# Performance work log

Measured on AMD Instinct MI355X. Metric: run time of the kernel, lower is better.

## Reference

```python
import jax, jax.numpy as jnp
import numpy as np

NEURONS = 512
CHANNELS = 384
H, W = 13, 13
BATCH = 512


def setup_inputs() -> dict:
    key = jax.random.key(0)
    kx, ks, kd, kb = jax.random.split(key, 4)
    x = jax.random.normal(kx, (BATCH, CHANNELS, H, W), dtype=jnp.float32)
    W_s = jax.random.normal(ks, (NEURONS, H, W), dtype=jnp.float32)      # spatial readout per neuron
    W_d = jax.random.normal(kd, (NEURONS, CHANNELS), dtype=jnp.float32)  # channel readout (squeezed 1x1 conv kernel)
    W_b = jax.random.normal(kb, (1, NEURONS), dtype=jnp.float32)
    return {"x": x, "W_s": W_s, "W_d": W_d, "W_b": W_b}


def reference(x, W_s, W_d, W_b):
    # Original: out = einsum('bchw,nhw->bnchw') -> per-neuron 1x1 conv with W_d[n] -> sum over (c,h,w) -> + W_b
    # Mathematically: out[b,n] = sum_{c,h,w} x[b,c,h,w] * W_s[n,h,w] * W_d[n,c] + W_b[0,n]
    # Factorized into two contractions, avoiding the (b,n,c,h,w) intermediate.
    pooled = jnp.einsum('bchw,nhw->bnc', x, W_s)   # spatial weighted pooling: [B, N, C]
    out = jnp.einsum('bnc,nc->bn', pooled, W_d)    # channel readout: [B, N]
    return out + W_b
```

## Files before the change

kernel.cpp:

```cpp
#include <hip/hip_runtime.h>


#define B_   512
#define C_   384
#define N_   512
#define HW_  169
#define CT   128
#define SXR  200

#define WSF_ELEMS  ((size_t)32 * 6 * 64 * 8)
#define WDF_ELEMS  ((size_t)24 * 32 * 64 * 4)
#define PART_ELEMS ((size_t)3 * B_ * N_)

typedef __bf16 bf16x8 __attribute__((ext_vector_type(8)));
typedef float f32x4  __attribute__((ext_vector_type(4)));
typedef float f32x4u __attribute__((ext_vector_type(4), aligned(4)));
typedef unsigned u32x4 __attribute__((ext_vector_type(4)));

__device__ __forceinline__ __bf16 f2bf(float f) {
  union { float f; unsigned u; } v; v.f = f;
  unsigned r = (v.u + 0x7FFFu + ((v.u >> 16) & 1u)) >> 16;
  unsigned short s = (unsigned short)r;
  return __builtin_bit_cast(__bf16, s);
}

__device__ __forceinline__ unsigned pack_trunc(float a, float b) {
  return __builtin_amdgcn_perm(__builtin_bit_cast(unsigned, b),
                               __builtin_bit_cast(unsigned, a), 0x07060302u);
}

__global__ __launch_bounds__(256)
void prep_aux_kernel(const float* __restrict__ Ws,
                     const float* __restrict__ Wd,
                     __bf16* __restrict__ wsf,
                     float* __restrict__ wdf) {
  int t = blockIdx.x * 256 + threadIdx.x;
  if (t < 12288) {
    int lane = t & 63;
    int fr   = t >> 6;
    int kb   = fr % 6;
    int nm   = fr / 6;
    int n    = nm * 16 + (lane & 15);
    int k0   = kb * 32 + (lane >> 4) * 8;
    const float* src = Ws + (size_t)n * HW_;
    bf16x8 v;
    #pragma unroll
    for (int j = 0; j < 8; ++j) {
      int k = k0 + j;
      float f = (k < HW_) ? src[k] : 0.f;
      v[j] = f2bf(f);
    }
    *(bf16x8*)(wsf + (size_t)t * 8) = v;
  } else {
    int t2 = t - 12288;
    int lane = t2 & 63;
    int fr   = t2 >> 6;
    int nm   = fr & 31;
    int cm   = fr >> 5;
    int n    = nm * 16 + (lane & 15);
    int c0   = cm * 16 + (lane >> 4) * 4;
    f32x4 w = *(const f32x4u*)(Wd + (size_t)n * C_ + c0);
    *(f32x4*)(wdf + (size_t)t2 * 4) = w;
  }
}

__global__ __launch_bounds__(256, 4)
void conv_part(const float* __restrict__ x,
               const __bf16* __restrict__ wsf,
               const float* __restrict__ wdf,
               float* __restrict__ part) {
  __shared__ float red[4 * 512];

  const int tid  = threadIdx.x;
  const int id    = blockIdx.x;
  const int slot  = id & 7;
  const int t8    = id >> 3;
  const int c_blk = t8 % 3;
  const int b     = (t8 / 3) * 8 + slot;

  const int lane  = tid & 63;
  const int wv    = tid >> 6;
  const int lrow  = lane & 15;
  const int lquad = lane >> 4;

  bf16x8 a[2][6];
  #pragma unroll
  for (int mi = 0; mi < 2; ++mi) {
    const float* rp = x + ((size_t)b * C_ + (size_t)c_blk * CT + wv * 32 + mi * 16 + lrow) * HW_;
    #pragma unroll
    for (int kb = 0; kb < 6; ++kb) {
      const int k0 = kb * 32 + lquad * 8;
      float v0, v1, v2, v3, v4, v5, v6, v7;
      if (kb < 5 || k0 + 7 < HW_) {
        f32x4u t0 = *(const f32x4u*)(rp + k0);
        f32x4u t1 = *(const f32x4u*)(rp + k0 + 4);
        v0 = t0[0]; v1 = t0[1]; v2 = t0[2]; v3 = t0[3];
        v4 = t1[0]; v5 = t1[1]; v6 = t1[2]; v7 = t1[3];
      } else {
        v0 = (k0 + 0 < HW_) ? rp[k0 + 0] : 0.f;
        v1 = v2 = v3 = v4 = v5 = v6 = v7 = 0.f;
      }
      u32x4 pk;
      pk.x = pack_trunc(v0, v1);
      pk.y = pack_trunc(v2, v3);
      pk.z = pack_trunc(v4, v5);
      pk.w = pack_trunc(v6, v7);
      a[mi][kb] = __builtin_bit_cast(bf16x8, pk);
    }
  }

  const int cm0 = c_blk * 8 + wv * 2;
  const __bf16* bb = wsf + (size_t)lane * 8;
  const float*  wb = wdf + (size_t)lane * 4;
  const f32x4 zero = {0.f, 0.f, 0.f, 0.f};

  #pragma unroll 1
  for (int nf = 0; nf < 32; ++nf) {
    bf16x8 bfr[6];
    #pragma unroll
    for (int kb = 0; kb < 6; ++kb)
      bfr[kb] = *(const bf16x8*)(bb + ((size_t)nf * 6 + kb) * 512);

    f32x4 acc[2] = {zero, zero};
    #pragma unroll
    for (int kb = 0; kb < 6; ++kb)
      #pragma unroll
      for (int mi = 0; mi < 2; ++mi)
        acc[mi] = __builtin_amdgcn_mfma_f32_16x16x32_bf16(
            a[mi][kb], bfr[kb], acc[mi], 0, 0, 0);

    float t = 0.f;
    #pragma unroll
    for (int mi = 0; mi < 2; ++mi) {
      const f32x4 w = *(const f32x4*)(wb + (((size_t)(cm0 + mi) * 32 + nf) * 256));
      t += acc[mi][0] * w[0] + acc[mi][1] * w[1]
         + acc[mi][2] * w[2] + acc[mi][3] * w[3];
    }
    t += __shfl_xor(t, 16, 64);
    t += __shfl_xor(t, 32, 64);
    if (lane < 16)
      red[wv * 512 + nf * 16 + lrow] = t;
  }
  __syncthreads();

  float* pb = part + ((size_t)c_blk * B_ + b) * N_;
  #pragma unroll
  for (int r = 0; r < 2; ++r) {
    const int n = r * 256 + tid;
    float v = red[n] + red[512 + n] + red[1024 + n] + red[1536 + n];
    pb[n] = v;
  }
}

__global__ __launch_bounds__(256)
void reduce_part(const float* __restrict__ part,
                 const float* __restrict__ Wb,
                 float* __restrict__ out) {
  const size_t S = (size_t)B_ * N_;
  int idx = (blockIdx.x * 256 + threadIdx.x) * 4;
  f32x4 a0 = *(const f32x4u*)(part + idx);
  f32x4 a1 = *(const f32x4u*)(part + S + idx);
  f32x4 a2 = *(const f32x4u*)(part + 2 * S + idx);
  f32x4 wb = *(const f32x4u*)(Wb + (idx & (N_ - 1)));
  f32x4 r;
  #pragma unroll
  for (int i = 0; i < 4; ++i)
    r[i] = a0[i] + a1[i] + a2[i] + wb[i];
  *(f32x4*)(out + idx) = r;
}

__global__ __launch_bounds__(256, 3)
void conv_fused_v8(const float* __restrict__ x,
                   const __bf16* __restrict__ wsf,
                   const float* __restrict__ wdf,
                   const float* __restrict__ Wb,
                   float* __restrict__ out) {
  __shared__ __align__(16) __bf16 Xs[CT * SXR];
  __shared__ float red[4][64];

  const int tid  = threadIdx.x;
  const int id    = blockIdx.x;
  const int slot  = id & 7;
  const int t8    = id >> 3;
  const int c_blk = t8 % 3;
  const int b     = (t8 / 3) * 8 + slot;

  const int lane  = tid & 63;
  const int wv    = tid >> 6;
  const int cq    = (wv >> 1) * 64;
  const int nq    = (wv & 1) * 64;
  const int lrow  = lane & 15;
  const int lquad = lane >> 4;

  const float* src = x + ((size_t)b * C_ + (size_t)c_blk * CT) * HW_;
  #pragma unroll 4
  for (int p = 0; p < 24; ++p) {
    int i   = p * 256 + tid;
    int row = i / 48;
    int ch  = i - row * 48;
    const float* bp = src + row * HW_ + ch * 4;
    float v0 = 0.f, v1 = 0.f, v2 = 0.f, v3 = 0.f;
    if (ch < 42) {
      f32x4u t = *(const f32x4u*)bp;
      v0 = t[0]; v1 = t[1]; v2 = t[2]; v3 = t[3];
    } else if (ch == 42) {
      v0 = bp[0];
    }
    unsigned d0 = pack_trunc(v0, v1);
    unsigned d1 = pack_trunc(v2, v3);
    uint2 d; d.x = d0; d.y = d1;
    *(uint2*)&Xs[row * SXR + ch * 4] = d;
  }
  __syncthreads();

  const int cm0 = c_blk * 8 + (cq >> 4);

  #pragma unroll 1
  for (int nb = 0; nb < 4; ++nb) {
    const int nm0 = nb * 8 + (nq >> 4);
    const __bf16* bbase = wsf + ((size_t)nm0 * 6) * 512 + (size_t)lane * 8;

    const f32x4 zero = {0.f, 0.f, 0.f, 0.f};
    f32x4 acc[4][4];
    #pragma unroll
    for (int mi = 0; mi < 4; ++mi)
      #pragma unroll
      for (int ni = 0; ni < 4; ++ni)
        acc[mi][ni] = zero;

    #pragma unroll
    for (int kb = 0; kb < 6; ++kb) {
      bf16x8 afr[4], bfr[4];
      #pragma unroll
      for (int mi = 0; mi < 4; ++mi)
        afr[mi] = *(const bf16x8*)&Xs[(cq + mi * 16 + lrow) * SXR + kb * 32 + lquad * 8];
      #pragma unroll
      for (int ni = 0; ni < 4; ++ni)
        bfr[ni] = *(const bf16x8*)(bbase + ((size_t)ni * 6 + kb) * 512);
      #pragma unroll
      for (int mi = 0; mi < 4; ++mi)
        #pragma unroll
        for (int ni = 0; ni < 4; ++ni)
          acc[mi][ni] = __builtin_amdgcn_mfma_f32_16x16x32_bf16(
              afr[mi], bfr[ni], acc[mi][ni], 0, 0, 0);
    }

    float s[4] = {0.f, 0.f, 0.f, 0.f};
    #pragma unroll
    for (int ni = 0; ni < 4; ++ni) {
      #pragma unroll
      for (int mi = 0; mi < 4; ++mi) {
        const f32x4 w = *(const f32x4*)(wdf +
            (((size_t)(cm0 + mi) * 32 + (nm0 + ni)) * 64 + lane) * 4);
        s[ni] += acc[mi][ni][0] * w[0] + acc[mi][ni][1] * w[1]
               + acc[mi][ni][2] * w[2] + acc[mi][ni][3] * w[3];
      }
    }

    #pragma unroll
    for (int ni = 0; ni < 4; ++ni) {
      s[ni] += __shfl_xor(s[ni], 16, 64);
      s[ni] += __shfl_xor(s[ni], 32, 64);
    }
    if (lane < 16) {
      #pragma unroll
      for (int ni = 0; ni < 4; ++ni)
        red[wv][ni * 16 + lrow] = s[ni];
    }
    __syncthreads();

    if (tid < 128) {
      const int half = tid >> 6;
      const int idx  = tid & 63;
      const int n    = nb * 128 + tid;
      float v = red[half][idx] + red[half + 2][idx];
      if (c_blk == 0) v += Wb[n];
      atomicAdd(&out[(size_t)b * N_ + n], v);
    }
    __syncthreads();
  }
}


#define LDSS 104
#define KCH  96
#define NT   128

__global__ __launch_bounds__(256)
void conv_main_fallback(const float* __restrict__ x,
                        const float* __restrict__ Ws_g,
                        const float* __restrict__ Wd,
                        const float* __restrict__ Wb,
                        float* __restrict__ out) {
  __shared__ __align__(16) __bf16 Xs[CT][LDSS];
  __shared__ __align__(16) __bf16 Ws[NT][LDSS];

  const int tid   = threadIdx.x;
  const int n_blk = blockIdx.x;
  const int c_blk = blockIdx.y;
  const int b     = blockIdx.z;
  const int c0 = c_blk * CT;
  const int n0 = n_blk * NT;
  const int lane  = tid & 63;
  const int wv    = tid >> 6;
  const int cq    = (wv >> 1) * 64;
  const int nq    = (wv & 1) * 64;
  const int lrow  = lane & 15;
  const int lquad = lane >> 4;

  const f32x4 zero = {0.f, 0.f, 0.f, 0.f};
  f32x4 acc[4][4];
  #pragma unroll
  for (int mi = 0; mi < 4; ++mi)
    #pragma unroll
    for (int ni = 0; ni < 4; ++ni)
      acc[mi][ni] = zero;

  const float* xb  = x    + (size_t)b  * (C_ * HW_) + (size_t)c0 * HW_;
  const float* wsb = Ws_g + (size_t)n0 * HW_;

  for (int ch = 0; ch < 2; ++ch) {
    const int k0 = ch * KCH;
    __syncthreads();
    for (int e = tid; e < CT * KCH; e += 256) {
      int r   = e / KCH;
      int col = e - r * KCH;
      int k   = k0 + col;
      float vx = 0.f, vw = 0.f;
      if (k < HW_) {
        vx = xb [r * HW_ + k];
        vw = wsb[r * HW_ + k];
      }
      Xs[r][col] = f2bf(vx);
      Ws[r][col] = f2bf(vw);
    }
    __syncthreads();

    #pragma unroll
    for (int ks = 0; ks < 3; ++ks) {
      const int kc = ks * 32 + lquad * 8;
      bf16x8 afr[4], bfr[4];
      #pragma unroll
      for (int mi = 0; mi < 4; ++mi)
        afr[mi] = *(const bf16x8*)&Xs[cq + mi * 16 + lrow][kc];
      #pragma unroll
      for (int ni = 0; ni < 4; ++ni)
        bfr[ni] = *(const bf16x8*)&Ws[nq + ni * 16 + lrow][kc];
      #pragma unroll
      for (int mi = 0; mi < 4; ++mi)
        #pragma unroll
        for (int ni = 0; ni < 4; ++ni)
          acc[mi][ni] = __builtin_amdgcn_mfma_f32_16x16x32_bf16(
              afr[mi], bfr[ni], acc[mi][ni], 0, 0, 0);
    }
  }

  #pragma unroll
  for (int ni = 0; ni < 4; ++ni) {
    const int n = n0 + nq + ni * 16 + lrow;
    float sv = 0.f;
    #pragma unroll
    for (int mi = 0; mi < 4; ++mi) {
      const int cbase = c0 + cq + mi * 16 + lquad * 4;
      #pragma unroll
      for (int i = 0; i < 4; ++i)
        sv += acc[mi][ni][i] * Wd[(size_t)n * C_ + (cbase + i)];
    }
    sv += __shfl_xor(sv, 16, 64);
    sv += __shfl_xor(sv, 32, 64);
    if (lane < 16) {
      if (c_blk == 0 && cq == 0) sv += Wb[n];
      atomicAdd(&out[(size_t)b * N_ + n], sv);
    }
  }
}

extern "C" void kernel_launch(void* const* d_in, const int* in_sizes, int n_in,
                              void* d_out, int out_size, void* d_ws, size_t ws_size,
                              hipStream_t stream) {
  const float* x   = (const float*)d_in[0];
  const float* Wsp = (const float*)d_in[1];
  const float* Wd  = (const float*)d_in[2];
  const float* Wb  = (const float*)d_in[3];
  float* out = (float*)d_out;

  const size_t need_basic = WSF_ELEMS * sizeof(__bf16) + WDF_ELEMS * sizeof(float);
  const size_t need_full  = need_basic + PART_ELEMS * sizeof(float);

  if (ws_size >= need_full) {
    __bf16* wsf  = (__bf16*)d_ws;
    float*  wdf  = (float*)(wsf + WSF_ELEMS);
    float*  partb = wdf + WDF_ELEMS;

    prep_aux_kernel<<<240, 256, 0, stream>>>(Wsp, Wd, wsf, wdf);
    conv_part<<<1536, 256, 0, stream>>>(x, wsf, wdf, partb);
    reduce_part<<<256, 256, 0, stream>>>(partb, Wb, out);
  } else if (ws_size >= need_basic) {
    __bf16* wsf = (__bf16*)d_ws;
    float*  wdf = (float*)(wsf + WSF_ELEMS);

    hipMemsetAsync(d_out, 0, (size_t)out_size * sizeof(float), stream);
    prep_aux_kernel<<<240, 256, 0, stream>>>(Wsp, Wd, wsf, wdf);
    conv_fused_v8<<<1536, 256, 0, stream>>>(x, wsf, wdf, Wb, out);
  } else {
    hipMemsetAsync(d_out, 0, (size_t)out_size * sizeof(float), stream);
    dim3 grid(N_ / NT, C_ / CT, B_);
    conv_main_fallback<<<grid, 256, 0, stream>>>(x, Wsp, Wd, Wb, out);
  }
}
```

Baseline: 249.1 us.

## Process two batch rows per block to reuse spatial and channel weight fragments

Each conv_part block now handles two batch elements instead of one, so every loaded W_s fragment and W_d vector feeds twice as many MFMAs. The grid is halved to 768 blocks. The shuffle reduction drops one xor step and writes to a larger padded LDS buffer with 8 partial rows per batch, which are summed at the end. This doubles the register footprint of the A fragments, so launch bounds are lowered from 4 to 3 blocks per SM, trading occupancy and parallelism for weight reuse.

```diff
diff --git a/kernel.cpp b/kernel.cpp
--- a/kernel.cpp
+++ b/kernel.cpp
@@ -7,6 +7,7 @@
 #define HW_  169
 #define CT   128
 #define SXR  200
+#define RSTR 516
 
 #define WSF_ELEMS  ((size_t)32 * 6 * 64 * 8)
 #define WDF_ELEMS  ((size_t)24 * 32 * 64 * 4)
@@ -64,48 +65,53 @@
   }
 }
 
-__global__ __launch_bounds__(256, 4)
+__global__ __launch_bounds__(256, 3)
 void conv_part(const float* __restrict__ x,
                const __bf16* __restrict__ wsf,
                const float* __restrict__ wdf,
                float* __restrict__ part) {
-  __shared__ float red[4 * 512];
+  __shared__ float red[2 * 8 * RSTR];
 
   const int tid  = threadIdx.x;
   const int id    = blockIdx.x;
   const int slot  = id & 7;
   const int t8    = id >> 3;
   const int c_blk = t8 % 3;
-  const int b     = (t8 / 3) * 8 + slot;
+  const int bp    = (t8 / 3) * 8 + slot;
+  const int b0    = bp * 2;
 
   const int lane  = tid & 63;
   const int wv    = tid >> 6;
   const int lrow  = lane & 15;
   const int lquad = lane >> 4;
 
-  bf16x8 a[2][6];
+  bf16x8 a[2][2][6];
   #pragma unroll
-  for (int mi = 0; mi < 2; ++mi) {
-    const float* rp = x + ((size_t)b * C_ + (size_t)c_blk * CT + wv * 32 + mi * 16 + lrow) * HW_;
-    #pragma unroll
-    for (int kb = 0; kb < 6; ++kb) {
-      const int k0 = kb * 32 + lquad * 8;
-      float v0, v1, v2, v3, v4, v5, v6, v7;
-      if (kb < 5 || k0 + 7 < HW_) {
-        f32x4u t0 = *(const f32x4u*)(rp + k0);
-        f32x4u t1 = *(const f32x4u*)(rp + k0 + 4);
-        v0 = t0[0]; v1 = t0[1]; v2 = t0[2]; v3 = t0[3];
-        v4 = t1[0]; v5 = t1[1]; v6 = t1[2]; v7 = t1[3];
-      } else {
-        v0 = (k0 + 0 < HW_) ? rp[k0 + 0] : 0.f;
-        v1 = v2 = v3 = v4 = v5 = v6 = v7 = 0.f;
+  for (int bi = 0; bi < 2; ++bi) {
+    #pragma unroll
+    for (int mi = 0; mi < 2; ++mi) {
+      const float* rp = x + ((size_t)(b0 + bi) * C_ + (size_t)c_blk * CT
+                             + wv * 32 + mi * 16 + lrow) * HW_;
+      #pragma unroll
+      for (int kb = 0; kb < 6; ++kb) {
+        const int k0 = kb * 32 + lquad * 8;
+        float v0, v1, v2, v3, v4, v5, v6, v7;
+        if (kb < 5 || k0 + 7 < HW_) {
+          f32x4u t0 = *(const f32x4u*)(rp + k0);
+          f32x4u t1 = *(const f32x4u*)(rp + k0 + 4);
+          v0 = t0[0]; v1 = t0[1]; v2 = t0[2]; v3 = t0[3];
+          v4 = t1[0]; v5 = t1[1]; v6 = t1[2]; v7 = t1[3];
+        } else {
+          v0 = (k0 + 0 < HW_) ? rp[k0 + 0] : 0.f;
+          v1 = v2 = v3 = v4 = v5 = v6 = v7 = 0.f;
+        }
+        u32x4 pk;
+        pk.x = pack_trunc(v0, v1);
+        pk.y = pack_trunc(v2, v3);
+        pk.z = pack_trunc(v4, v5);
+        pk.w = pack_trunc(v6, v7);
+        a[bi][mi][kb] = __builtin_bit_cast(bf16x8, pk);
       }
-      u32x4 pk;
-      pk.x = pack_trunc(v0, v1);
-      pk.y = pack_trunc(v2, v3);
-      pk.z = pack_trunc(v4, v5);
-      pk.w = pack_trunc(v6, v7);
-      a[mi][kb] = __builtin_bit_cast(bf16x8, pk);
     }
   }
 
@@ -113,6 +119,8 @@
   const __bf16* bb = wsf + (size_t)lane * 8;
   const float*  wb = wdf + (size_t)lane * 4;
   const f32x4 zero = {0.f, 0.f, 0.f, 0.f};
+  const int rrow = wv * 2 + (lquad >> 1);
+  const bool wlane = ((lquad & 1) == 0);
 
   #pragma unroll 1
   for (int nf = 0; nf < 32; ++nf) {
@@ -121,34 +129,47 @@
     for (int kb = 0; kb < 6; ++kb)
       bfr[kb] = *(const bf16x8*)(bb + ((size_t)nf * 6 + kb) * 512);
 
-    f32x4 acc[2] = {zero, zero};
+    f32x4 w[2];
+    #pragma unroll
+    for (int mi = 0; mi < 2; ++mi)
+      w[mi] = *(const f32x4*)(wb + (((size_t)(cm0 + mi) * 32 + nf) * 256));
+
+    f32x4 acc[2][2] = {{zero, zero}, {zero, zero}};
     #pragma unroll
     for (int kb = 0; kb < 6; ++kb)
       #pragma unroll
+      for (int bi = 0; bi < 2; ++bi)
+        #pragma unroll
+        for (int mi = 0; mi < 2; ++mi)
+          acc[bi][mi] = __builtin_amdgcn_mfma_f32_16x16x32_bf16(
+              a[bi][mi][kb], bfr[kb], acc[bi][mi], 0, 0, 0);
+
+    #pragma unroll
+    for (int bi = 0; bi < 2; ++bi) {
+      float t = 0.f;
+      #pragma unroll
       for (int mi = 0; mi < 2; ++mi)
-        acc[mi] = __builtin_amdgcn_mfma_f32_16x16x32_bf16(
-            a[mi][kb], bfr[kb], acc[mi], 0, 0, 0);
-
-    float t = 0.f;
-    #pragma unroll
-    for (int mi = 0; mi < 2; ++mi) {
-      const f32x4 w = *(const f32x4*)(wb + (((size_t)(cm0 + mi) * 32 + nf) * 256));
-      t += acc[mi][0] * w[0] + acc[mi][1] * w[1]
-         + acc[mi][2] * w[2] + acc[mi][3] * w[3];
-    }
-    t += __shfl_xor(t, 16, 64);
-    t += __shfl_xor(t, 32, 64);
-    if (lane < 16)
-      red[wv * 512 + nf * 16 + lrow] = t;
+        t += acc[bi][mi][0] * w[mi][0] + acc[bi][mi][1] * w[mi][1]
+           + acc[bi][mi][2] * w[mi][2] + acc[bi][mi][3] * w[mi][3];
+      t += __shfl_xor(t, 16, 64);
+      if (wlane)
+        red[(bi * 8 + rrow) * RSTR + nf * 16 + lrow] = t;
+    }
   }
   __syncthreads();
 
-  float* pb = part + ((size_t)c_blk * B_ + b) * N_;
+  float* pb = part + ((size_t)c_blk * B_ + b0) * N_;
   #pragma unroll
   for (int r = 0; r < 2; ++r) {
     const int n = r * 256 + tid;
-    float v = red[n] + red[512 + n] + red[1024 + n] + red[1536 + n];
-    pb[n] = v;
+    float v0 = 0.f, v1 = 0.f;
+    #pragma unroll
+    for (int s = 0; s < 8; ++s) {
+      v0 += red[s * RSTR + n];
+      v1 += red[(8 + s) * RSTR + n];
+    }
+    pb[n] = v0;
+    pb[N_ + n] = v1;
   }
 }
 
@@ -393,7 +414,7 @@
     float*  partb = wdf + WDF_ELEMS;
 
     prep_aux_kernel<<<240, 256, 0, stream>>>(Wsp, Wd, wsf, wdf);
-    conv_part<<<1536, 256, 0, stream>>>(x, wsf, wdf, partb);
+    conv_part<<<768, 256, 0, stream>>>(x, wsf, wdf, partb);
     reduce_part<<<256, 256, 0, stream>>>(partb, Wb, out);
   } else if (ws_size >= need_basic) {
     __bf16* wsf = (__bf16*)d_ws;
```

Result: faster. 242.7 us (-2.6%).

## Stage spatial-weight fragments through double-buffered LDS with async global-to-LDS loads

Applied to the files above, without the earlier changes.

The bf16 spatial-weight fragments are now loaded cooperatively into a double-buffered shared-memory tile with global_load_lds. Each chunk covers four neuron tiles, and the next chunk is prefetched while MFMAs run on the current one. Before, every wave read the same fragments straight from global memory. The channel weights for a whole chunk are also loaded up front. The cost is 48KB of LDS per block and a drop in the occupancy hint from 4 to 2 blocks, plus a block-wide barrier per chunk.

```diff
diff --git a/kernel.cpp b/kernel.cpp
--- a/kernel.cpp
+++ b/kernel.cpp
@@ -27,6 +27,13 @@
 __device__ __forceinline__ unsigned pack_trunc(float a, float b) {
   return __builtin_amdgcn_perm(__builtin_bit_cast(unsigned, b),
                                __builtin_bit_cast(unsigned, a), 0x07060302u);
+}
+
+__device__ __forceinline__ void gload_lds16(const __bf16* g, __bf16* l) {
+  __builtin_amdgcn_global_load_lds(
+      (const __attribute__((address_space(1))) unsigned*)(g),
+      (__attribute__((address_space(3))) unsigned*)(l),
+      16, 0, 0);
 }
 
 __global__ __launch_bounds__(256)
@@ -64,11 +71,12 @@
   }
 }
 
-__global__ __launch_bounds__(256, 4)
+__global__ __launch_bounds__(256, 2)
 void conv_part(const float* __restrict__ x,
                const __bf16* __restrict__ wsf,
                const float* __restrict__ wdf,
                float* __restrict__ part) {
+  __shared__ __align__(16) __bf16 Bs[2][24 * 512];
   __shared__ float red[4 * 512];
 
   const int tid  = threadIdx.x;
@@ -110,38 +118,67 @@
   }
 
   const int cm0 = c_blk * 8 + wv * 2;
-  const __bf16* bb = wsf + (size_t)lane * 8;
-  const float*  wb = wdf + (size_t)lane * 4;
+  const float* wb = wdf + (size_t)lane * 4;
   const f32x4 zero = {0.f, 0.f, 0.f, 0.f};
+  float* rbase = red + wv * 512;
+
+  {
+    const __bf16* g = wsf + ((size_t)(wv * 6) * 512) + (size_t)lane * 8;
+    __bf16* l = &Bs[0][(wv * 6) * 512];
+    #pragma unroll
+    for (int j = 0; j < 6; ++j)
+      gload_lds16(g + j * 512, l + j * 512);
+  }
+  __syncthreads();
 
   #pragma unroll 1
-  for (int nf = 0; nf < 32; ++nf) {
-    bf16x8 bfr[6];
-    #pragma unroll
-    for (int kb = 0; kb < 6; ++kb)
-      bfr[kb] = *(const bf16x8*)(bb + ((size_t)nf * 6 + kb) * 512);
-
-    f32x4 acc[2] = {zero, zero};
-    #pragma unroll
-    for (int kb = 0; kb < 6; ++kb)
+  for (int ch = 0; ch < 8; ++ch) {
+    const int buf = ch & 1;
+
+    f32x4 w[4][2];
+    #pragma unroll
+    for (int nfi = 0; nfi < 4; ++nfi)
       #pragma unroll
       for (int mi = 0; mi < 2; ++mi)
-        acc[mi] = __builtin_amdgcn_mfma_f32_16x16x32_bf16(
-            a[mi][kb], bfr[kb], acc[mi], 0, 0, 0);
-
-    float t = 0.f;
-    #pragma unroll
-    for (int mi = 0; mi < 2; ++mi) {
-      const f32x4 w = *(const f32x4*)(wb + (((size_t)(cm0 + mi) * 32 + nf) * 256));
-      t += acc[mi][0] * w[0] + acc[mi][1] * w[1]
-         + acc[mi][2] * w[2] + acc[mi][3] * w[3];
-    }
-    t += __shfl_xor(t, 16, 64);
-    t += __shfl_xor(t, 32, 64);
-    if (lane < 16)
-      red[wv * 512 + nf * 16 + lrow] = t;
-  }
-  __syncthreads();
+        w[nfi][mi] = *(const f32x4*)(wb +
+            (((size_t)(cm0 + mi) * 32 + (ch * 4 + nfi)) * 256));
+
+    if (ch < 7) {
+      const __bf16* g = wsf + ((size_t)((ch + 1) * 24 + wv * 6) * 512) + (size_t)lane * 8;
+      __bf16* l = &Bs[buf ^ 1][(wv * 6) * 512];
+      #pragma unroll
+      for (int j = 0; j < 6; ++j)
+        gload_lds16(g + j * 512, l + j * 512);
+    }
+
+    #pragma unroll
+    for (int nfi = 0; nfi < 4; ++nfi) {
+      bf16x8 bfr[6];
+      #pragma unroll
+      for (int kb = 0; kb < 6; ++kb)
+        bfr[kb] = *(const bf16x8*)&Bs[buf][(nfi * 6 + kb) * 512 + lane * 8];
+
+      f32x4 acc[2] = {zero, zero};
+      #pragma unroll
+      for (int kb = 0; kb < 6; ++kb)
+        #pragma unroll
+        for (int mi = 0; mi < 2; ++mi)
+          acc[mi] = __builtin_amdgcn_mfma_f32_16x16x32_bf16(
+              a[mi][kb], bfr[kb], acc[mi], 0, 0, 0);
+
+      float t = 0.f;
+      #pragma unroll
+      for (int mi = 0; mi < 2; ++mi)
+        t += acc[mi][0] * w[nfi][mi][0] + acc[mi][1] * w[nfi][mi][1]
+           + acc[mi][2] * w[nfi][mi][2] + acc[mi][3] * w[nfi][mi][3];
+      t += __shfl_xor(t, 16, 64);
+      t += __shfl_xor(t, 32, 64);
+      if (lane < 16)
+        rbase[(ch * 4 + nfi) * 16 + lrow] = t;
+    }
+
+    __syncthreads();
+  }
 
   float* pb = part + ((size_t)c_blk * B_ + b) * N_;
   #pragma unroll
```

Result: faster. 235.6 us (-5.4%).
